# Performance work log

Measured on AMD Instinct MI355X. Metric: run time of the kernel, lower is better.

The kernel has to match this reference:

```python
import jax, jax.numpy as jnp
import numpy as np

LN_EPS = 1e-5
EPS = 1e-3
C_S, C_Z, C_H = 256, 128, 32
B, S, R = 1, 128, 256


def setup_inputs() -> dict:
    key = jax.random.key(0)
    ks = jax.random.split(key, 8)
    m = jax.random.normal(ks[0], (B, S, R, C_S), dtype=jnp.float32)
    mask = jax.random.uniform(ks[1], (B, S, R), dtype=jnp.float32)
    ln_w = jnp.ones((C_S,), jnp.float32)
    ln_b = jnp.zeros((C_S,), jnp.float32)
    # store linear weights as [in, out] for direct einsum/matmul
    w1 = jax.random.normal(ks[2], (C_S, C_H), jnp.float32) / np.sqrt(C_S)
    b1 = jnp.zeros((C_H,), jnp.float32)
    w2 = jax.random.normal(ks[3], (C_S, C_H), jnp.float32) / np.sqrt(C_S)
    b2 = jnp.zeros((C_H,), jnp.float32)
    w_out = jax.random.normal(ks[4], (C_H * C_H, C_Z), jnp.float32) / np.sqrt(C_H * C_H)
    b_out = jnp.zeros((C_Z,), jnp.float32)
    return {"m": m, "mask": mask, "ln_w": ln_w, "ln_b": ln_b,
            "w1": w1, "b1": b1, "w2": w2, "b2": b2,
            "w_out": w_out, "b_out": b_out}


def reference(m, mask, ln_w, ln_b, w1, b1, w2, b2, w_out, b_out):
    # LayerNorm over C_s
    mu = jnp.mean(m, axis=-1, keepdims=True)
    var = jnp.var(m, axis=-1, keepdims=True)
    mh = (m - mu) * jax.lax.rsqrt(var + LN_EPS) * ln_w + ln_b
    mk = mask[..., None]                      # [B,S,R,1]
    a = (mh @ w1 + b1) * mk                   # [B,S,R,H]
    b = (mh @ w2 + b2) * mk                   # [B,S,R,H]
    a = jnp.swapaxes(a, -2, -3)               # [B,R,S,H]
    b = jnp.swapaxes(b, -2, -3)               # [B,R,S,H]
    # outer-product mean: contract over N_seq -> [B,R,R,H,H]
    outer = jnp.einsum('bish,bjsk->bijhk', a, b)
    outer = outer.reshape(outer.shape[:-2] + (C_H * C_H,))
    outer = outer @ w_out + b_out             # [B,R,R,C_z]
    norm = jnp.einsum('bsi,bsj->bij', mask, mask)[..., None]  # [B,R,R,1]
    return outer / (EPS + norm)
```

## Files before the change

### kernel.cpp

```cpp
#include <hip/hip_runtime.h>
#include <hip/hip_bf16.h>

typedef short v8s __attribute__((ext_vector_type(8)));
typedef float v4f __attribute__((ext_vector_type(4)));
typedef float v16f __attribute__((ext_vector_type(16)));
typedef float v2f __attribute__((ext_vector_type(2)));

#define LN_EPS 1e-5f
#define EPS_N 1e-3f

__device__ __forceinline__ unsigned short f2bf(float f) {
    __hip_bfloat16 h = __float2bfloat16(f);
    return __builtin_bit_cast(unsigned short, h);
}
__device__ __forceinline__ unsigned int pk2(float a, float b) {
    return (unsigned)f2bf(a) | ((unsigned)f2bf(b) << 16);
}


__global__ __launch_bounds__(256) void k0_prep(
    const float* __restrict__ mask,
    const float* __restrict__ w1, const float* __restrict__ w2,
    const float* __restrict__ w_out,
    unsigned short* __restrict__ wt,
    unsigned short* __restrict__ w_out_f,
    float* __restrict__ inv_norm) {
    const int b = blockIdx.x, t = threadIdx.x;
    if (b < 32) {
        const int f = b * 256 + t;
        const int c = f >> 5, h = f & 31;
        wt[h * 256 + c] = f2bf(w1[f]);
    } else if (b < 64) {
        const int f = (b - 32) * 256 + t;
        const int c = f >> 5, h = f & 31;
        wt[(32 + h) * 256 + c] = f2bf(w2[f]);
    }
    #pragma unroll
    for (int e2 = 0; e2 < 2; ++e2) {
        const int f = b * 512 + e2 * 256 + t;
        const int h = f >> 12, k = (f >> 7) & 31, z = f & 127;
        const int k2 = (h >> 2) * 128 + k * 4 + (h & 3);
        const int tt = k2 >> 4, halfv = (k2 >> 3) & 1, e8 = k2 & 7;
        const int zhv = z >> 6, l31v = (z & 63) >> 1, ee = z & 1;
        const int d = (((tt * 4 + zhv * 2 + ee) * 2 + halfv) * 32 + l31v) * 8 + e8;
        w_out_f[d] = f2bf(w_out[f]);
    }
    float a0 = 0.f, a1 = 0.f, a2 = 0.f, a3 = 0.f;
    #pragma unroll 4
    for (int s = 0; s < 128; s += 4) {
        a0 += mask[(s + 0) * 256 + b] * mask[(s + 0) * 256 + t];
        a1 += mask[(s + 1) * 256 + b] * mask[(s + 1) * 256 + t];
        a2 += mask[(s + 2) * 256 + b] * mask[(s + 2) * 256 + t];
        a3 += mask[(s + 3) * 256 + b] * mask[(s + 3) * 256 + t];
    }
    inv_norm[b * 256 + t] = 1.0f / (EPS_N + (a0 + a1) + (a2 + a3));
}

__global__ __launch_bounds__(256, 4) void k1_lnproj(
    const float* __restrict__ m, const float* __restrict__ mask,
    const float* __restrict__ ln_w, const float* __restrict__ ln_b,
    const float* __restrict__ b1, const float* __restrict__ b2,
    const unsigned short* __restrict__ wt,
    unsigned short* __restrict__ a_f, unsigned short* __restrict__ b_f) {
    __shared__ unsigned short mh[32 * 256];
    const int r = blockIdx.x, sq = blockIdx.y;
    const int tid = threadIdx.x;
    const int w = tid >> 6, l = tid & 63;
    const int quad = l >> 4, l15 = l & 15;

    const float4 lwv = *(const float4*)(ln_w + l * 4);
    const float4 lbv = *(const float4*)(ln_b + l * 4);

    const int sg0 = sq * 32 + w * 8;
    float4 v[8];
    #pragma unroll
    for (int it = 0; it < 8; ++it)
        v[it] = *(const float4*)(m + (size_t)((sg0 + it) * 256 + r) * 256 + (l << 2));
    #pragma unroll
    for (int it = 0; it < 8; ++it) {
        const float4 x = v[it];
        float sum = x.x + x.y + x.z + x.w;
        float sq2 = x.x * x.x + x.y * x.y + x.z * x.z + x.w * x.w;
        for (int off = 32; off; off >>= 1) {
            sum += __shfl_xor(sum, off);
            sq2 += __shfl_xor(sq2, off);
        }
        const float mu   = sum * (1.f / 256.f);
        const float var  = sq2 * (1.f / 256.f) - mu * mu;
        const float rstd = rsqrtf(var + LN_EPS);
        const unsigned int p0 = pk2((x.x - mu) * rstd * lwv.x + lbv.x,
                                    (x.y - mu) * rstd * lwv.y + lbv.y);
        const unsigned int p1 = pk2((x.z - mu) * rstd * lwv.z + lbv.z,
                                    (x.w - mu) * rstd * lwv.w + lbv.w);
        const int sl = w * 8 + it;
        const int addr = sl * 256 + (((l >> 1) ^ (sl & 31)) << 3) + ((l & 1) << 2);
        *(uint2*)(&mh[addr]) = make_uint2(p0, p1);
    }
    __syncthreads();

    const int mt = w >> 1, nh = w & 1;
    v4f acc[2];
    const v4f z4 = {0.f, 0.f, 0.f, 0.f};
    acc[0] = z4; acc[1] = z4;

    const int row = mt * 16 + l15;
    #pragma unroll
    for (int kb = 0; kb < 8; ++kb) {
        const v8s af = *(const v8s*)(&mh[row * 256 + (((kb * 4 + quad) ^ (row & 31)) << 3)]);
        #pragma unroll
        for (int tn = 0; tn < 2; ++tn) {
            const v8s bf = *(const v8s*)(wt + (nh * 32 + tn * 16 + l15) * 256 + kb * 32 + quad * 8);
            acc[tn] = __builtin_amdgcn_mfma_f32_16x16x32_bf16(af, bf, acc[tn], 0, 0, 0);
        }
    }

    const int s0 = sq * 32 + mt * 16 + quad * 4;
    const int kb_s = s0 >> 4, half_s = (s0 >> 3) & 1, e0 = s0 & 7;
    float mk[4];
    #pragma unroll
    for (int u = 0; u < 4; ++u) mk[u] = mask[(s0 + u) * 256 + r];
    #pragma unroll
    for (int tn = 0; tn < 2; ++tn) {
        const int h2 = nh * 32 + tn * 16 + l15;
        const float bias = (h2 < 32) ? b1[h2] : b2[h2 - 32];
        unsigned short* dst = (h2 < 32) ? a_f : b_f;
        const int h = h2 & 31;
        const v4f f = acc[tn];
        const unsigned int q0 = pk2((f[0] + bias) * mk[0], (f[1] + bias) * mk[1]);
        const unsigned int q1 = pk2((f[2] + bias) * mk[2], (f[3] + bias) * mk[3]);
        const int addr = ((r * 8 + kb_s) * 64 + half_s * 32 + h) * 8 + e0;
        *(uint2*)(dst + addr) = make_uint2(q0, q1);
    }
}

#define SYNC_LGKM0 asm volatile("s_waitcnt lgkmcnt(0)" ::: "memory")
#define SYNC_VM(n) asm volatile("s_waitcnt vmcnt(" #n ")" ::: "memory")
#define BARRIER()  { __builtin_amdgcn_s_barrier(); __builtin_amdgcn_sched_barrier(0); }

__global__ __launch_bounds__(512, 2) void k2_main(
    const unsigned short* __restrict__ a_f,
    const unsigned short* __restrict__ b_f,
    const unsigned short* __restrict__ w_out_f,
    const float* __restrict__ inv_norm,
    const float* __restrict__ b_out,
    float* __restrict__ out) {
    __shared__ __align__(16) unsigned char smem[163840];
    unsigned short* Bs = (unsigned short*)smem;
    unsigned short* P  = (unsigned short*)(smem + 65536);
    unsigned int*  red = (unsigned int*)(smem + 131072);

    const int g = blockIdx.x;
    const int ib = g >> 2, jq0 = (g & 3) * 16;
    const int tid = threadIdx.x, w = tid >> 6, l = tid & 63;
    const int l31 = l & 31, half = l >> 5;
    const int wm = w >> 1, wn = w & 1;
    const int zh = w >> 2, kq = w & 3;

    v8s wfr[16][2];
    #pragma unroll
    for (int tl = 0; tl < 16; ++tl) {
        #pragma unroll
        for (int e = 0; e < 2; ++e)
            wfr[tl][e] = *(const v8s*)(w_out_f + ((kq * 16 + tl) * 4 + zh * 2 + e) * 512 + l * 8);
    }
    v8s aP[8];
    {
        const unsigned short* ab = a_f + (size_t)(ib * 4 + wm) * 4096 + l * 8;
        #pragma unroll
        for (int kb = 0; kb < 8; ++kb)
            aP[kb] = *(const v8s*)(ab + kb * 512);
    }
    const float bo0 = b_out[zh * 64 + 2 * l31];
    const float bo1 = b_out[zh * 64 + 2 * l31 + 1];

    auto dma = [&](int q, int hsel) {
        const char* gb = (const char*)b_f + (size_t)(jq0 + q) * 32768;
        #pragma unroll
        for (int it = 0; it < 4; ++it) {
            const int c = w * 4 + it;
            __builtin_amdgcn_global_load_lds((const unsigned int*)(gb + c * 1024 + l * 16),
                                             (unsigned int*)((char*)Bs + hsel * 32768 + c * 1024), 16, 0, 0);
        }
    };
    __builtin_amdgcn_sched_barrier(0);
    dma(0, 0);
    dma(1, 1);

    const v16f z16 = {0.f,0.f,0.f,0.f,0.f,0.f,0.f,0.f,0.f,0.f,0.f,0.f,0.f,0.f,0.f,0.f};

    auto stage2 = [&](int hsel) {
        v16f acc2[2];
        acc2[0] = z16; acc2[1] = z16;
        const char* Bh = (const char*)Bs + hsel * 32768;
        __builtin_amdgcn_s_setprio(1);
        #pragma unroll
        for (int kb = 0; kb < 8; ++kb) {
            const v8s b0 = *(const v8s*)(Bh + (wn * 2 + 0) * 8192 + kb * 1024 + l * 16);
            const v8s b1 = *(const v8s*)(Bh + (wn * 2 + 1) * 8192 + kb * 1024 + l * 16);
            acc2[0] = __builtin_amdgcn_mfma_f32_32x32x16_bf16(aP[kb], b0, acc2[0], 0, 0, 0);
            acc2[1] = __builtin_amdgcn_mfma_f32_32x32x16_bf16(aP[kb], b1, acc2[1], 0, 0, 0);
        }
        __builtin_amdgcn_s_setprio(0);
        #pragma unroll
        for (int nj = 0; nj < 2; ++nj) {
            const int p = wm * 8 + hsel * 4 + wn * 2 + nj;
            const int esw = 2 * (p & 15);
            const v16f f = acc2[nj];
            #pragma unroll
            for (int q = 0; q < 4; ++q) {
                const unsigned int lo = pk2(f[4 * q + 0], f[4 * q + 1]);
                const unsigned int hi = pk2(f[4 * q + 2], f[4 * q + 3]);
                const int u8 = (2 * q + half) * 32 + l31;
                *(uint2*)(P + p * 1024 + ((u8 ^ esw) << 2)) = make_uint2(lo, hi);
            }
        }
    };

    auto stage3 = [&]() {
        v16f acc3[2];
        acc3[0] = z16; acc3[1] = z16;
        __builtin_amdgcn_s_setprio(1);
        #pragma unroll
        for (int tl = 0; tl < 16; ++tl) {
            const int t2 = kq * 16 + tl;
            const int u8 = t2 * 4 + half * 2;
            const v8s pa = *(const v8s*)(P + l31 * 1024 + ((u8 ^ (2 * (l31 & 15))) << 2));
            acc3[0] = __builtin_amdgcn_mfma_f32_32x32x16_bf16(pa, wfr[tl][0], acc3[0], 0, 0, 0);
            acc3[1] = __builtin_amdgcn_mfma_f32_32x32x16_bf16(pa, wfr[tl][1], acc3[1], 0, 0, 0);
        }
        __builtin_amdgcn_s_setprio(0);
        #pragma unroll
        for (int q = 0; q < 4; ++q) {
            #pragma unroll
            for (int u = 0; u < 4; ++u) {
                const int rr = 4 * q + u;
                const int p = u + 8 * q + 4 * half;
                red[w * 1024 + p * 32 + l31] = pk2(acc3[0][rr], acc3[1][rr]);
            }
        }
    };

    auto epilogue = [&](int jbx) {
        const int pq = w & 3;
        #pragma unroll
        for (int pi = 0; pi < 4; ++pi) {
            const int p = pq * 8 + half * 4 + pi;
            const int gi = ib * 4 + (p >> 3);
            const int gj = jbx * 8 + (p & 7);
            const float inv = inv_norm[gi * 256 + gj];
            float s0 = 0.f, s1 = 0.f;
            #pragma unroll
            for (int kk = 0; kk < 4; ++kk) {
                const unsigned int u = red[(zh * 4 + kk) * 1024 + p * 32 + l31];
                s0 += __builtin_bit_cast(float, u << 16);
                s1 += __builtin_bit_cast(float, u & 0xffff0000u);
            }
            v2f res;
            res.x = (s0 + bo0) * inv;
            res.y = (s1 + bo1) * inv;
            __builtin_nontemporal_store(res,
                (v2f*)(out + (size_t)(gi * 256 + gj) * 128 + zh * 64) + l31);
        }
    };

    #pragma unroll 1
    for (int blk = 0; blk < 8; ++blk) {
        SYNC_LGKM0;
        SYNC_VM(4);
        BARRIER();
        stage2(0);
        if (blk > 0) epilogue((g & 3) * 8 + blk - 1);
        SYNC_LGKM0;
        SYNC_VM(0);
        BARRIER();
        if (blk < 7) dma(2 * blk + 2, 0);

        stage2(1);
        SYNC_LGKM0;
        BARRIER();
        if (blk < 7) dma(2 * blk + 3, 1);
        stage3();
    }
    SYNC_LGKM0;
    BARRIER();
    epilogue((g & 3) * 8 + 7);
}

extern "C" void kernel_launch(void* const* d_in, const int* in_sizes, int n_in,
                              void* d_out, int out_size, void* d_ws, size_t ws_size,
                              hipStream_t stream) {
    const float* m     = (const float*)d_in[0];
    const float* mask  = (const float*)d_in[1];
    const float* ln_w  = (const float*)d_in[2];
    const float* ln_b  = (const float*)d_in[3];
    const float* w1    = (const float*)d_in[4];
    const float* b1    = (const float*)d_in[5];
    const float* w2    = (const float*)d_in[6];
    const float* b2    = (const float*)d_in[7];
    const float* w_out = (const float*)d_in[8];
    const float* b_out = (const float*)d_in[9];
    float* out = (float*)d_out;

    unsigned short* a_f      = (unsigned short*)d_ws;
    unsigned short* b_f      = a_f + 8192 * 128;
    unsigned short* w_out_f  = b_f + 8192 * 128;
    float*          inv_norm = (float*)(w_out_f + 128 * 1024);
    unsigned short* wt       = (unsigned short*)(inv_norm + 65536);

    k0_prep<<<256, 256, 0, stream>>>(mask, w1, w2, w_out, wt, w_out_f, inv_norm);
    k1_lnproj<<<dim3(256, 4), 256, 0, stream>>>(m, mask, ln_w, ln_b, b1, b2, wt, a_f, b_f);
    k2_main<<<256, 512, 0, stream>>>(a_f, b_f, w_out_f, inv_norm, b_out, out);
}
```

Before: 147.6 us.

## Load B operand directly from global memory instead of LDS double-buffering

Removes the async global-to-LDS DMA double buffer for the B tiles and has each wave read its B fragments straight from global memory (via L2/L1) inside the MFMA loop. This cuts LDS usage from 160KB to 96KB and drops several vmcnt waits and barriers. The trade-off is that global-load latency is no longer hidden by prefetching, so the MFMA loop may stall on memory unless occupancy or caching covers it. Barrier placement also changes, with an extra barrier after stage3.

```diff
diff --git a/kernel.cpp b/kernel.cpp
--- a/kernel.cpp
+++ b/kernel.cpp
@@ -134,7 +134,6 @@
 }
 
 #define SYNC_LGKM0 asm volatile("s_waitcnt lgkmcnt(0)" ::: "memory")
-#define SYNC_VM(n) asm volatile("s_waitcnt vmcnt(" #n ")" ::: "memory")
 #define BARRIER()  { __builtin_amdgcn_s_barrier(); __builtin_amdgcn_sched_barrier(0); }
 
 __global__ __launch_bounds__(512, 2) void k2_main(
@@ -144,13 +143,12 @@
     const float* __restrict__ inv_norm,
     const float* __restrict__ b_out,
     float* __restrict__ out) {
-    __shared__ __align__(16) unsigned char smem[163840];
-    unsigned short* Bs = (unsigned short*)smem;
-    unsigned short* P  = (unsigned short*)(smem + 65536);
-    unsigned int*  red = (unsigned int*)(smem + 131072);
+    __shared__ __align__(16) unsigned char smem[98304];
+    unsigned short* P  = (unsigned short*)smem;
+    unsigned int*  red = (unsigned int*)(smem + 65536);
 
     const int g = blockIdx.x;
-    const int ib = g >> 2, jq0 = (g & 3) * 16;
+    const int ib = g >> 2, jb0 = (g & 3) * 8;
     const int tid = threadIdx.x, w = tid >> 6, l = tid & 63;
     const int l31 = l & 31, half = l >> 5;
     const int wm = w >> 1, wn = w & 1;
@@ -173,30 +171,17 @@
     const float bo0 = b_out[zh * 64 + 2 * l31];
     const float bo1 = b_out[zh * 64 + 2 * l31 + 1];
 
-    auto dma = [&](int q, int hsel) {
-        const char* gb = (const char*)b_f + (size_t)(jq0 + q) * 32768;
-        #pragma unroll
-        for (int it = 0; it < 4; ++it) {
-            const int c = w * 4 + it;
-            __builtin_amdgcn_global_load_lds((const unsigned int*)(gb + c * 1024 + l * 16),
-                                             (unsigned int*)((char*)Bs + hsel * 32768 + c * 1024), 16, 0, 0);
-        }
-    };
-    __builtin_amdgcn_sched_barrier(0);
-    dma(0, 0);
-    dma(1, 1);
-
     const v16f z16 = {0.f,0.f,0.f,0.f,0.f,0.f,0.f,0.f,0.f,0.f,0.f,0.f,0.f,0.f,0.f,0.f};
 
-    auto stage2 = [&](int hsel) {
+    auto stage2 = [&](int jbx, int hsel) {
         v16f acc2[2];
         acc2[0] = z16; acc2[1] = z16;
-        const char* Bh = (const char*)Bs + hsel * 32768;
+        const char* Bg = (const char*)b_f + (size_t)(jbx * 8 + hsel * 4) * 8192;
         __builtin_amdgcn_s_setprio(1);
         #pragma unroll
         for (int kb = 0; kb < 8; ++kb) {
-            const v8s b0 = *(const v8s*)(Bh + (wn * 2 + 0) * 8192 + kb * 1024 + l * 16);
-            const v8s b1 = *(const v8s*)(Bh + (wn * 2 + 1) * 8192 + kb * 1024 + l * 16);
+            const v8s b0 = *(const v8s*)(Bg + (wn * 2 + 0) * 8192 + kb * 1024 + l * 16);
+            const v8s b1 = *(const v8s*)(Bg + (wn * 2 + 1) * 8192 + kb * 1024 + l * 16);
             acc2[0] = __builtin_amdgcn_mfma_f32_32x32x16_bf16(aP[kb], b0, acc2[0], 0, 0, 0);
             acc2[1] = __builtin_amdgcn_mfma_f32_32x32x16_bf16(aP[kb], b1, acc2[1], 0, 0, 0);
         }
@@ -265,25 +250,19 @@
 
     #pragma unroll 1
     for (int blk = 0; blk < 8; ++blk) {
-        SYNC_LGKM0;
-        SYNC_VM(4);
-        BARRIER();
-        stage2(0);
-        if (blk > 0) epilogue((g & 3) * 8 + blk - 1);
-        SYNC_LGKM0;
-        SYNC_VM(0);
-        BARRIER();
-        if (blk < 7) dma(2 * blk + 2, 0);
-
-        stage2(1);
+        const int jbx = jb0 + blk;
+        stage2(jbx, 0);
+        __builtin_amdgcn_sched_barrier(0);
+        if (blk > 0) epilogue(jbx - 1);
+        __builtin_amdgcn_sched_barrier(0);
+        stage2(jbx, 1);
         SYNC_LGKM0;
         BARRIER();
-        if (blk < 7) dma(2 * blk + 3, 1);
         stage3();
-    }
-    SYNC_LGKM0;
-    BARRIER();
-    epilogue((g & 3) * 8 + 7);
+        SYNC_LGKM0;
+        BARRIER();
+    }
+    epilogue(jb0 + 7);
 }
 
 extern "C" void kernel_launch(void* const* d_in, const int* in_sizes, int n_in,
```

Result: slower. 189.2 us (+28.2%).
